# Kernel tuning notes

Hardware: AMD Instinct MI355X
Metric: run time of the kernel (lower is better)

Reference implementation:

```python
import jax, jax.numpy as jnp
import numpy as np

N_TOKEN = 100000
D = 1024  # d_embed == d_model == d_proj
CUTOFFS = [0, 20000, 60000, 100000]  # cutoff_ends
N_SEQ = 2048


def setup_inputs() -> dict:
    key = jax.random.key(0)
    ks = jax.random.split(key, 20)
    w = lambda k, s: jax.random.normal(k, s, dtype=jnp.float32) * 0.02
    return {
        "x": jax.random.randint(ks[0], (N_SEQ,), 0, N_TOKEN),
        "labels": jax.random.randint(ks[1], (N_SEQ,), 0, N_TOKEN),
        # adaptive embedding tables (d_emb_i = 1024 / 4**i) and projections [d_proj, d_emb_i]
        "emb_w0": w(ks[2], (20000, 1024)),
        "emb_w1": w(ks[3], (40000, 256)),
        "emb_w2": w(ks[4], (40000, 64)),
        "emb_proj0": w(ks[5], (1024, 1024)),
        "emb_proj1": w(ks[6], (1024, 256)),
        "emb_proj2": w(ks[7], (1024, 64)),
        # adaptive softmax output layers + projections
        "out_w0": w(ks[8], (20000, 1024)),
        "out_b0": jnp.zeros((20000,), jnp.float32),
        "out_w1": w(ks[9], (40000, 256)),
        "out_b1": jnp.zeros((40000,), jnp.float32),
        "out_w2": w(ks[10], (40000, 64)),
        "out_b2": jnp.zeros((40000,), jnp.float32),
        "out_proj0": w(ks[11], (1024, 1024)),
        "out_proj1": w(ks[12], (1024, 256)),
        "out_proj2": w(ks[13], (1024, 64)),
        # cluster head tokens (one per tail cluster)
        "cluster_w": w(ks[14], (2, 1024)),
        "cluster_b": jnp.zeros((2,), jnp.float32),
    }


def _forward(x, labels,
             emb_w0, emb_w1, emb_w2, emb_proj0, emb_proj1, emb_proj2,
             out_w0, out_b0, out_w1, out_b1, out_w2, out_b2,
             out_proj0, out_proj1, out_proj2, cluster_w, cluster_b):
    scale = jnp.asarray(D ** 0.5, jnp.float32)
    # AdaptiveEmbedding (div_val>1): per-cluster embed -> project to d_proj, scatter by range.
    # Equivalent vectorized form: build the full projected table once, then gather.
    table = jnp.concatenate([
        emb_w0 @ emb_proj0.T,   # [20000, D]
        emb_w1 @ emb_proj1.T,   # [40000, D]
        emb_w2 @ emb_proj2.T,   # [40000, D]
    ], axis=0)                   # [N_TOKEN, D]
    hidden = table[x] * scale    # [N, D]

    n = hidden.shape[0]
    rows = jnp.arange(n)

    # Head: cluster-0 vocab + one logit per tail cluster.
    head_w = jnp.concatenate([out_w0, cluster_w], axis=0)   # [20002, D]
    head_b = jnp.concatenate([out_b0, cluster_b], axis=0)   # [20002]
    head_logit = (hidden @ out_proj0) @ head_w.T + head_b   # [N, 20002]
    head_lp = jax.nn.log_softmax(head_logit, axis=-1)
    head_size = head_lp.shape[1]

    # Cluster 0: direct lookup in the head.
    lp0 = head_lp[rows, jnp.clip(labels, 0, CUTOFFS[1] - 1)]

    # Tail clusters: dense per-cluster log-softmax, gathered at shifted target,
    # plus the head cluster-token logprob (original TXL uses column -i).
    def tail(w, b, proj, i):
        l, r = CUTOFFS[i], CUTOFFS[i + 1]
        tail_lp = jax.nn.log_softmax((hidden @ proj) @ w.T + b, axis=-1)  # [N, r-l]
        t = jnp.clip(labels - l, 0, r - l - 1)
        return head_lp[:, head_size - i] + tail_lp[rows, t]

    lp1 = tail(out_w1, out_b1, out_proj1, 1)
    lp2 = tail(out_w2, out_b2, out_proj2, 2)

    logprob = jnp.where(labels < CUTOFFS[1], lp0,
               jnp.where(labels < CUTOFFS[2], lp1, lp2))
    return -logprob  # nll, [N]


def reference(x, labels,
              emb_w0, emb_w1, emb_w2, emb_proj0, emb_proj1, emb_proj2,
              out_w0, out_b0, out_w1, out_b1, out_w2, out_b2,
              out_proj0, out_proj1, out_proj2, cluster_w, cluster_b):
    return _forward(x, labels,
                    emb_w0, emb_w1, emb_w2, emb_proj0, emb_proj1, emb_proj2,
                    out_w0, out_b0, out_w1, out_b1, out_w2, out_b2,
                    out_proj0, out_proj1, out_proj2, cluster_w, cluster_b)
```

## Files before the change

### kernel.cpp

```cpp
#include <hip/hip_runtime.h>

typedef _Float16 f16x8 __attribute__((ext_vector_type(8)));
typedef _Float16 f16x4 __attribute__((ext_vector_type(4)));
typedef float f32x4 __attribute__((ext_vector_type(4)));
typedef int i32x8 __attribute__((ext_vector_type(8)));
typedef unsigned char u8;

#define DEVI __device__ __forceinline__

constexpr int NROWS = 2048;
constexpr int HEADV = 20002;
constexpr int HEADP = 20480;
constexpr int NCBH  = 160;
constexpr int PSTH  = 160;
constexpr int VT    = 40000;
constexpr int VTP   = 40320;
constexpr int NCBT  = 315;
constexpr int PSTT  = 320;

DEVI void glds16(const void* g, void* l) {
  __builtin_amdgcn_global_load_lds((const __attribute__((address_space(1))) unsigned int*)g,
                                   (__attribute__((address_space(3))) unsigned int*)l,
                                   16, 0, 0);
}

#define SIG(r) (((r) >> 1) & 7)

DEVI unsigned int to_e4m3(float f) {
  unsigned u = __float_as_uint(f);
  unsigned s = (u >> 24) & 0x80u;
  float a = fabsf(f);
  if (!(a < 448.f)) return s | 0x7E;
  if (a < 0.00097656f) return s;
  int exp = (int)((u >> 23) & 0xFF) - 127;
  int qexp = exp < -6 ? -6 : exp;
  int n = __float2int_rn(a * exp2f((float)(3 - qexp)));
  if (n >= 16) { qexp++; n = 8; }
  return s | (unsigned)(n < 8 ? n : (((qexp + 7) << 3) | (n - 8)));
}

DEVI float fr8(unsigned b) {
  unsigned e = (b >> 3) & 15u, m = b & 7u;
  float v;
  if (e) v = __uint_as_float(((e + 120u) << 23) | (m << 20));
  else   v = (float)m * 0.001953125f;
  return (b & 0x80u) ? -v : v;
}

__global__ void prep_par(const int* __restrict__ x, const int* __restrict__ labels,
                         int* cl, int* headcol, int* tailpos, int* pos1, int* pos2,
                         int* L1, int* L2, int* T0, int* T1, int* T2, int* counts)
{
  int n = blockIdx.x * 256 + threadIdx.x;
  int l = labels[n];
  int c = l < 20000 ? 0 : (l < 60000 ? 1 : 2);
  cl[n] = c;
  headcol[n] = c == 0 ? l : (c == 1 ? 20001 : 20000);
  tailpos[n] = c == 1 ? l - 20000 : (c == 2 ? l - 60000 : 0);
  if (c == 1) { int s = atomicAdd(&counts[0], 1); pos1[n] = s; L1[s] = n; }
  else if (c == 2) { int s = atomicAdd(&counts[1], 1); pos2[n] = s; L2[s] = n; }
  int t = x[n];
  int tc = t < 20000 ? 0 : (t < 60000 ? 1 : 2);
  int s = atomicAdd(&counts[2 + tc], 1);
  (tc == 0 ? T0 : tc == 1 ? T1 : T2)[s] = n;
}

constexpr int PB_A = HEADP * 1024 / 8 / 256;
constexpr int PB_B = PB_A + VTP * 256 / 8 / 256;
constexpr int PB_C = PB_B + VTP * 128 / 8 / 256;
constexpr int PB_D = PB_C + 1024;
constexpr int PB_E = PB_D + 256;
constexpr int PB_F = PB_E + 64;
constexpr int PB_G = PB_F + 1024;
constexpr int PB_H = PB_G + 256;
constexpr int PB_I = PB_H + 128;

DEVI void cvt_f16(const float* src, _Float16* dst, int vb, int tid) {
  int g = vb * 256 + tid;
  float4 v = *(const float4*)(src + (size_t)g * 4);
  f16x4 o = {(_Float16)v.x, (_Float16)v.y, (_Float16)v.z, (_Float16)v.w};
  *(f16x4*)(dst + (size_t)g * 4) = o;
}

DEVI void tr32(const float* in, _Float16* out, int C, int bx, int by, int tid) {
  __shared__ float tile[32][33];
  int c0 = bx * 32, r0 = by * 32;
  int tx = tid & 31, ty = tid >> 5;
  for (int i = 0; i < 4; i++) {
    int c = c0 + tx; int r = r0 + ty + i * 8;
    tile[ty + i * 8][tx] = (c < C) ? in[(size_t)r * C + c] : 0.f;
  }
  __syncthreads();
  for (int i = 0; i < 4; i++)
    out[(size_t)(c0 + ty + i * 8) * 1024 + r0 + tx] = (_Float16)tile[tx][ty + i * 8];
}

DEVI unsigned long pack8(const float* v) {
  unsigned long p = 0;
  #pragma unroll
  for (int j = 0; j < 8; j++) p |= (unsigned long)to_e4m3(v[j] * 64.f) << (8 * j);
  return p;
}

__global__ void fused_pack(const float* __restrict__ out_w0, const float* __restrict__ out_b0,
                           const float* __restrict__ cluster_w, const float* __restrict__ cluster_b,
                           const float* __restrict__ out_w1, const float* __restrict__ out_b1,
                           const float* __restrict__ out_w2, const float* __restrict__ out_b2,
                           const float* __restrict__ emb_proj0, const float* __restrict__ emb_proj1,
                           const float* __restrict__ emb_proj2,
                           const float* __restrict__ out_proj0, const float* __restrict__ out_proj1,
                           const float* __restrict__ out_proj2,
                           u8* headw, float* headb,
                           u8* w1q, float* b1p, u8* w2q, float* b2p,
                           _Float16* ep0f, _Float16* ep1f, _Float16* ep2f,
                           _Float16* op0T, _Float16* op1T, _Float16* op2T,
                           int* lists, int* counts)
{
  int bid = blockIdx.x, tid = threadIdx.x;
  int zi = bid * 256 + tid;
  if (zi < 5 * 2048) lists[zi] = 0;
  if (bid == 41 && tid < 8) counts[tid] = 0;
  if (bid < PB_A) {
    int g = bid * 256 + tid;
    int r = g >> 7, sl = g & 127;
    float v[8] = {};
    if (r < 20000) {
      *(float4*)v = *(const float4*)(out_w0 + (size_t)r * 1024 + sl * 8);
      *(float4*)(v + 4) = *(const float4*)(out_w0 + (size_t)r * 1024 + sl * 8 + 4);
    } else if (r < 20002) {
      *(float4*)v = *(const float4*)(cluster_w + (size_t)(r - 20000) * 1024 + sl * 8);
      *(float4*)(v + 4) = *(const float4*)(cluster_w + (size_t)(r - 20000) * 1024 + sl * 8 + 4);
    }
    *(unsigned long*)(headw + (size_t)r * 1024 + ((sl ^ SIG(r)) << 3)) = pack8(v);
    if (g < HEADP) headb[g] = g < 20000 ? out_b0[g] : (g < HEADV ? cluster_b[g - 20000] : -1e30f);
  } else if (bid < PB_B) {
    int g = (bid - PB_A) * 256 + tid;
    int r = g >> 5, sl = g & 31;
    float v[8] = {};
    if (r < VT) {
      *(float4*)v = *(const float4*)(out_w1 + (size_t)r * 256 + sl * 8);
      *(float4*)(v + 4) = *(const float4*)(out_w1 + (size_t)r * 256 + sl * 8 + 4);
    }
    *(unsigned long*)(w1q + (size_t)r * 256 + ((sl ^ SIG(r)) << 3)) = pack8(v);
    if (g < VTP) b1p[g] = g < VT ? out_b1[g] : -1e30f;
  } else if (bid < PB_C) {
    int g = (bid - PB_B) * 256 + tid;
    int r = g >> 4, sl = g & 15;
    float v[8] = {};
    if (r < VT && sl < 8) {
      *(float4*)v = *(const float4*)(out_w2 + (size_t)r * 64 + sl * 8);
      *(float4*)(v + 4) = *(const float4*)(out_w2 + (size_t)r * 64 + sl * 8 + 4);
    }
    *(unsigned long*)(w2q + (size_t)r * 128 + ((sl ^ SIG(r)) << 3)) = pack8(v);
    if (g < VTP) b2p[g] = g < VT ? out_b2[g] : -1e30f;
  } else if (bid < PB_D) { cvt_f16(emb_proj0, ep0f, bid - PB_C, tid); }
  else if (bid < PB_E) { cvt_f16(emb_proj1, ep1f, bid - PB_D, tid); }
  else if (bid < PB_F) { cvt_f16(emb_proj2, ep2f, bid - PB_E, tid); }
  else if (bid < PB_G) { int l = bid - PB_F; tr32(out_proj0, op0T, 1024, l & 31, l >> 5, tid); }
  else if (bid < PB_H) { int l = bid - PB_G; tr32(out_proj1, op1T, 256, l & 7, l >> 3, tid); }
  else                 { int l = bid - PB_H; tr32(out_proj2, op2T, 64, l & 3, l >> 2, tid); }
}

DEVI void gat(const float* emb, const int* x, const int* list, _Float16* dst,
              int tbase, int vmax, int log2E, int vb, int tid) {
  int g = vb * 256 + tid;
  int r = g >> (log2E - 2);
  int e4 = (g & ((1 << (log2E - 2)) - 1)) << 2;
  int n = list[r];
  int tl = x[n] - tbase;
  tl = tl < 0 ? 0 : (tl >= vmax ? vmax - 1 : tl);
  float4 v = *(const float4*)(emb + ((size_t)tl << log2E) + e4);
  f16x4 o = {(_Float16)(v.x * 32.f), (_Float16)(v.y * 32.f),
             (_Float16)(v.z * 32.f), (_Float16)(v.w * 32.f)};
  *(f16x4*)(dst + ((size_t)r << log2E) + e4) = o;
}

__global__ void fused_gather(const float* __restrict__ emb_w0, const float* __restrict__ emb_w1,
                             const float* __restrict__ emb_w2, const int* __restrict__ x,
                             const int* __restrict__ T0, const int* __restrict__ T1,
                             const int* __restrict__ T2,
                             _Float16* E0, _Float16* E1, _Float16* E2)
{
  int bid = blockIdx.x, tid = threadIdx.x;
  if (bid < 2048)      gat(emb_w0, x, T0, E0, 0, 20000, 10, bid, tid);
  else if (bid < 2560) gat(emb_w1, x, T1, E1, 20000, 40000, 8, bid - 2048, tid);
  else                 gat(emb_w2, x, T2, E2, 60000, 40000, 6, bid - 2560, tid);
}

struct Seg128 {
  const _Float16* A; int lda;
  const _Float16* Wm; int ldw;
  _Float16* C; int ldc; int Nvalid;
  u8* Cq; int ldq;
  const int* amap; const int* cmap; const int* cnt;
  int K; int nblk;
};

DEVI void gemm128_body(const Seg128& s, int rb, int cb) {
  int valid = s.cnt ? *s.cnt : NROWS;
  if (rb * 128 >= valid) return;
  __shared__ __attribute__((aligned(16))) _Float16 As[128 * 32];
  __shared__ __attribute__((aligned(16))) _Float16 Ws[128 * 32];
  int tid = threadIdx.x;
  int lane = tid & 63, wid = tid >> 6;
  int wr = wid >> 1, wc = wid & 1;
  int sr = wid * 32 + (lane >> 2);
  int arow0 = rb * 128 + sr, arow1 = arow0 + 16;
  if (s.amap) { arow0 = s.amap[arow0]; arow1 = s.amap[arow1]; }
  int ko = (lane & 3) * 8;
  const _Float16* ag0 = s.A + (size_t)arow0 * s.lda + ko;
  const _Float16* ag1 = s.A + (size_t)arow1 * s.lda + ko;
  const _Float16* wg0 = s.Wm + (size_t)(cb * 128 + sr) * s.ldw + ko;
  const _Float16* wg1 = wg0 + (size_t)16 * s.ldw;
  _Float16* as0 = As + (wid * 32) * 32;
  _Float16* as1 = as0 + 16 * 32;
  _Float16* ws0 = Ws + (wid * 32) * 32;
  _Float16* ws1 = ws0 + 16 * 32;
  f32x4 acc[4][4] = {};
  int lr = lane & 15, lk = (lane >> 4) * 8;
  const int nk = s.K >> 5;
  for (int kt = 0; kt < nk; ++kt) {
    int kofs = kt * 32;
    glds16(ag0 + kofs, as0);
    glds16(ag1 + kofs, as1);
    glds16(wg0 + kofs, ws0);
    glds16(wg1 + kofs, ws1);
    __syncthreads();
    f16x8 af[4], bf[4];
    #pragma unroll
    for (int mi = 0; mi < 4; mi++)
      af[mi] = *(const f16x8*)(As + (wr * 64 + mi * 16 + lr) * 32 + lk);
    #pragma unroll
    for (int ni = 0; ni < 4; ni++)
      bf[ni] = *(const f16x8*)(Ws + (wc * 64 + ni * 16 + lr) * 32 + lk);
    #pragma unroll
    for (int mi = 0; mi < 4; mi++)
      #pragma unroll
      for (int ni = 0; ni < 4; ni++)
        acc[mi][ni] = __builtin_amdgcn_mfma_f32_16x16x32_f16(af[mi], bf[ni], acc[mi][ni], 0, 0, 0);
    __syncthreads();
  }
  #pragma unroll
  for (int mi = 0; mi < 4; mi++) {
    #pragma unroll
    for (int j = 0; j < 4; j++) {
      int rl = wr * 64 + mi * 16 + (lane >> 4) * 4 + j;
      int rg = rb * 128 + rl;
      if (rg >= valid) continue;
      int orow = s.cmap ? s.cmap[rg] : rg;
      #pragma unroll
      for (int ni = 0; ni < 4; ni++) {
        int col = cb * 128 + wc * 64 + ni * 16 + (lane & 15);
        if (col < s.Nvalid) {
          float v = acc[mi][ni][j];
          s.C[(size_t)orow * s.ldc + col] = (_Float16)v;
          if (s.Cq) {
            int sl = col >> 3;
            s.Cq[(size_t)orow * s.ldq + (((sl ^ SIG(orow)) << 3) | (col & 7))] = (u8)to_e4m3(v * 8.f);
          }
        }
      }
    }
  }
}

__global__ __launch_bounds__(256)
void gemm128_multi(Seg128 s0, Seg128 s1, Seg128 s2) {
  int b = blockIdx.x;
  if (b < s0.nblk)                    { gemm128_body(s0, b & 15, b >> 4); }
  else if (b < s0.nblk + s1.nblk)     { b -= s0.nblk; gemm128_body(s1, b & 15, b >> 4); }
  else                                { b -= s0.nblk + s1.nblk; gemm128_body(s2, b & 15, b >> 4); }
}

struct SegL {
  const u8* A; const u8* W; const float* bias; const int* cnt;
  float* pm; float* ps; int pstride; int K; int nrb; int nblk;
};

__global__ __launch_bounds__(256)
void gemm_lse8_multi(SegL s0, SegL s1, SegL s2)
{
  __shared__ __attribute__((aligned(16))) u8 As[16384];
  __shared__ __attribute__((aligned(16))) u8 Ws[16384];

  int b = blockIdx.x;
  SegL s;
  if (b < s0.nblk) s = s0;
  else if (b < s0.nblk + s1.nblk) { s = s1; b -= s0.nblk; }
  else { s = s2; b -= s0.nblk + s1.nblk; }

  int q = s.nblk >> 3;
  int w = (b & 7) * q + (b >> 3);
  int rb = w % s.nrb, cb = w / s.nrb;
  int valid = s.cnt ? *s.cnt : NROWS;
  if (rb * 128 >= valid) return;

  const int K = s.K;
  int tid = threadIdx.x;
  int lane = tid & 63, wid = tid >> 6;
  int wr = wid >> 1, wc = wid & 1;
  int lr = lane & 15, g = lane >> 4;

  const u8* aS[4]; const u8* bS[4]; int dL[4];
  #pragma unroll
  for (int i = 0; i < 4; ++i) {
    int c = tid + i * 256;
    int r = c >> 3, j = c & 7;
    aS[i] = s.A + (size_t)(rb * 128 + r) * K + j * 16;
    bS[i] = s.W + (size_t)((size_t)cb * 128 + r) * K + j * 16;
    dL[i] = c * 16;
  }

  int sig = (lr >> 1) & 7;
  int o0 = ((g * 4 + 0) ^ sig) << 3;
  int o1 = ((g * 4 + 1) ^ sig) << 3;
  int o2 = ((g * 4 + 2) ^ sig) << 3;
  int o3 = ((g * 4 + 3) ^ sig) << 3;
  int arow = (wr * 64 + lr) * 128;
  int brow = (wc * 64 + lr) * 128;

  f32x4 acc[4][4] = {};
  const int nk = K >> 7;

  union UV { i32x8 v; long l[4]; };
  for (int kt = 0; kt < nk; ++kt) {
    int k0 = kt * 128;
    #pragma unroll
    for (int i = 0; i < 4; ++i) glds16(aS[i] + k0, As + dL[i]);
    #pragma unroll
    for (int i = 0; i < 4; ++i) glds16(bS[i] + k0, Ws + dL[i]);
    __syncthreads();
    i32x8 bq[4];
    #pragma unroll
    for (int ni = 0; ni < 4; ++ni) {
      UV bv;
      const u8* bp = Ws + brow + ni * 2048;
      bv.l[0] = *(const long*)(bp + o0);
      bv.l[1] = *(const long*)(bp + o1);
      bv.l[2] = *(const long*)(bp + o2);
      bv.l[3] = *(const long*)(bp + o3);
      bq[ni] = bv.v;
    }
    #pragma unroll
    for (int mi = 0; mi < 4; ++mi) {
      UV av;
      const u8* ap = As + arow + mi * 2048;
      av.l[0] = *(const long*)(ap + o0);
      av.l[1] = *(const long*)(ap + o1);
      av.l[2] = *(const long*)(ap + o2);
      av.l[3] = *(const long*)(ap + o3);
      #pragma unroll
      for (int ni = 0; ni < 4; ++ni)
        acc[mi][ni] = __builtin_amdgcn_mfma_scale_f32_16x16x128_f8f6f4(
                        av.v, bq[ni], acc[mi][ni], 0, 0, 0, 127, 0, 127);
    }
    __syncthreads();
  }

  float* lm = (float*)As;
  float* lsm = lm + 256;
  float bv4[4];
  #pragma unroll
  for (int ni = 0; ni < 4; ++ni) bv4[ni] = s.bias[cb * 128 + wc * 64 + ni * 16 + lr];
  constexpr float INV = 1.f / 512.f;
  #pragma unroll
  for (int mi = 0; mi < 4; ++mi) {
    #pragma unroll
    for (int j = 0; j < 4; ++j) {
      float v0 = acc[mi][0][j] * INV + bv4[0];
      float v1 = acc[mi][1][j] * INV + bv4[1];
      float v2 = acc[mi][2][j] * INV + bv4[2];
      float v3 = acc[mi][3][j] * INV + bv4[3];
      float m = fmaxf(fmaxf(v0, v1), fmaxf(v2, v3));
      #pragma unroll
      for (int d = 1; d < 16; d <<= 1) m = fmaxf(m, __shfl_xor(m, d));
      float sm = __expf(v0 - m) + __expf(v1 - m) + __expf(v2 - m) + __expf(v3 - m);
      #pragma unroll
      for (int d = 1; d < 16; d <<= 1) sm += __shfl_xor(sm, d);
      if (lr == 0) {
        int row = wr * 64 + mi * 16 + g * 4 + j;
        lm[wc * 128 + row] = m; lsm[wc * 128 + row] = sm;
      }
    }
  }
  __syncthreads();
  if (tid < 128) {
    float m0 = lm[tid], m1 = lm[128 + tid];
    float M = fmaxf(m0, m1);
    float S = lsm[tid] * __expf(m0 - M) + lsm[128 + tid] * __expf(m1 - M);
    int gr = rb * 128 + tid;
    s.pm[(size_t)gr * s.pstride + cb] = M;
    s.ps[(size_t)gr * s.pstride + cb] = S;
  }
}

DEVI float lsew(const float* m, const float* s, int nb, int lane) {
  float M = -3e38f;
  for (int i = lane; i < nb; i += 64) M = fmaxf(M, m[i]);
  #pragma unroll
  for (int d = 1; d < 64; d <<= 1) M = fmaxf(M, __shfl_xor(M, d));
  float S = 0.f;
  for (int i = lane; i < nb; i += 64) S += s[i] * __expf(m[i] - M);
  #pragma unroll
  for (int d = 1; d < 64; d <<= 1) S += __shfl_xor(S, d);
  return M + __logf(S);
}

__global__ void finish_kernel(const _Float16* __restrict__ ph0, const u8* __restrict__ headw,
                              const float* __restrict__ headb,
                              const _Float16* __restrict__ ph1c, const u8* __restrict__ w1q,
                              const float* __restrict__ b1p,
                              const _Float16* __restrict__ ph2c, const u8* __restrict__ w2q,
                              const float* __restrict__ b2p,
                              const int* __restrict__ headcol, const int* __restrict__ tailpos,
                              const int* __restrict__ pos1, const int* __restrict__ pos2,
                              const int* __restrict__ cl,
                              const float* __restrict__ pmh, const float* __restrict__ psh,
                              const float* __restrict__ pm1, const float* __restrict__ ps1,
                              const float* __restrict__ pm2, const float* __restrict__ ps2,
                              float* __restrict__ out)
{
  int n = blockIdx.x;
  int tid = threadIdx.x, lane = tid & 63, wid = tid >> 6;
  __shared__ float sh[6];
  int c = cl[n];
  constexpr float IW = 1.f / 64.f;
  if (wid == 0) {
    int hc = headcol[n];
    const f16x8* a = (const f16x8*)(ph0 + (size_t)n * 1024 + lane * 16);
    float s = 0.f;
    #pragma unroll
    for (int u = 0; u < 2; u++) {
      int sl = lane * 2 + u;
      unsigned long wq = *(const unsigned long*)(headw + (size_t)hc * 1024 + (((sl ^ SIG(hc)) << 3)));
      f16x8 av = a[u];
      #pragma unroll
      for (int j = 0; j < 8; j++) s += (float)av[j] * fr8((unsigned)(wq >> (8 * j)) & 0xFFu);
    }
    #pragma unroll
    for (int d = 1; d < 64; d <<= 1) s += __shfl_xor(s, d);
    if (lane == 0) sh[0] = s * IW + headb[hc];
  } else if (wid == 1 && c == 1) {
    int p = pos1[n], t = tailpos[n];
    f16x4 av = *(const f16x4*)(ph1c + (size_t)p * 256 + lane * 4);
    int sl = lane >> 1;
    const u8* ww = w1q + (size_t)t * 256 + ((sl ^ SIG(t)) << 3) + (lane & 1) * 4;
    float s = (float)av[0] * fr8(ww[0]) + (float)av[1] * fr8(ww[1])
            + (float)av[2] * fr8(ww[2]) + (float)av[3] * fr8(ww[3]);
    #pragma unroll
    for (int d = 1; d < 64; d <<= 1) s += __shfl_xor(s, d);
    float l = lsew(pm1 + (size_t)p * PSTT, ps1 + (size_t)p * PSTT, NCBT, lane);
    if (lane == 0) { sh[1] = s * IW + b1p[t]; sh[4] = l; }
  } else if (wid == 2 && c == 2) {
    int p = pos2[n], t = tailpos[n];
    const _Float16* a = ph2c + (size_t)p * 128 + lane * 2;
    int sl = lane >> 2;
    const u8* ww = w2q + (size_t)t * 128 + ((sl ^ SIG(t)) << 3) + (lane & 3) * 2;
    float s = (float)a[0] * fr8(ww[0]) + (float)a[1] * fr8(ww[1]);
    #pragma unroll
    for (int d = 1; d < 64; d <<= 1) s += __shfl_xor(s, d);
    float l = lsew(pm2 + (size_t)p * PSTT, ps2 + (size_t)p * PSTT, NCBT, lane);
    if (lane == 0) { sh[2] = s * IW + b2p[t]; sh[5] = l; }
  } else if (wid == 3) {
    float l = lsew(pmh + (size_t)n * PSTH, psh + (size_t)n * PSTH, NCBH, lane);
    if (lane == 0) sh[3] = l;
  }
  __syncthreads();
  if (tid == 0) {
    float nll = sh[3] - sh[0];
    if (c == 1)      nll += sh[4] - sh[1];
    else if (c == 2) nll += sh[5] - sh[2];
    out[n] = nll;
  }
}

extern "C" void kernel_launch(void* const* d_in, const int* in_sizes, int n_in,
                              void* d_out, int out_size, void* d_ws, size_t ws_size,
                              hipStream_t stream)
{
  const int*   x         = (const int*)d_in[0];
  const int*   labels    = (const int*)d_in[1];
  const float* emb_w0    = (const float*)d_in[2];
  const float* emb_w1    = (const float*)d_in[3];
  const float* emb_w2    = (const float*)d_in[4];
  const float* emb_proj0 = (const float*)d_in[5];
  const float* emb_proj1 = (const float*)d_in[6];
  const float* emb_proj2 = (const float*)d_in[7];
  const float* out_w0    = (const float*)d_in[8];
  const float* out_b0    = (const float*)d_in[9];
  const float* out_w1    = (const float*)d_in[10];
  const float* out_b1    = (const float*)d_in[11];
  const float* out_w2    = (const float*)d_in[12];
  const float* out_b2    = (const float*)d_in[13];
  const float* out_proj0 = (const float*)d_in[14];
  const float* out_proj1 = (const float*)d_in[15];
  const float* out_proj2 = (const float*)d_in[16];
  const float* cluster_w = (const float*)d_in[17];
  const float* cluster_b = (const float*)d_in[18];
  float* out = (float*)d_out;

  char* ws = (char*)d_ws;
  size_t off = 0;
  auto alloc = [&](size_t bytes) -> void* {
    void* p = ws + off;
    off = (off + bytes + 255) & ~(size_t)255;
    return p;
  };
  u8*    headw = (u8*)alloc((size_t)HEADP * 1024);
  float* headb = (float*)alloc((size_t)HEADP * 4);
  u8*    w1q   = (u8*)alloc((size_t)VTP * 256);
  float* b1p   = (float*)alloc((size_t)VTP * 4);
  u8*    w2q   = (u8*)alloc((size_t)VTP * 128);
  float* b2p   = (float*)alloc((size_t)VTP * 4);
  _Float16* ep0f = (_Float16*)alloc((size_t)1024 * 1024 * 2);
  _Float16* ep1f = (_Float16*)alloc((size_t)1024 * 256 * 2);
  _Float16* ep2f = (_Float16*)alloc((size_t)1024 * 64 * 2);
  _Float16* op0T = (_Float16*)alloc((size_t)1024 * 1024 * 2);
  _Float16* op1T = (_Float16*)alloc((size_t)256 * 1024 * 2);
  _Float16* op2T = (_Float16*)alloc((size_t)128 * 1024 * 2);
  _Float16* E0   = (_Float16*)alloc((size_t)NROWS * 1024 * 2);
  _Float16* E1   = (_Float16*)alloc((size_t)NROWS * 256 * 2);
  _Float16* E2   = (_Float16*)alloc((size_t)NROWS * 64 * 2);
  _Float16* hid  = (_Float16*)alloc((size_t)NROWS * 1024 * 2);
  _Float16* ph0  = (_Float16*)alloc((size_t)NROWS * 1024 * 2);
  u8*       ph0q = (u8*)alloc((size_t)NROWS * 1024);
  _Float16* ph1c = (_Float16*)alloc((size_t)NROWS * 256 * 2);
  u8*       ph1q = (u8*)alloc((size_t)NROWS * 256);
  _Float16* ph2c = (_Float16*)alloc((size_t)NROWS * 128 * 2);
  u8*       ph2q = (u8*)alloc((size_t)NROWS * 128);
  float* pmh = (float*)alloc((size_t)NROWS * PSTH * 4);
  float* psh = (float*)alloc((size_t)NROWS * PSTH * 4);
  float* pm1 = (float*)alloc((size_t)NROWS * PSTT * 4);
  float* ps1 = (float*)alloc((size_t)NROWS * PSTT * 4);
  float* pm2 = (float*)alloc((size_t)NROWS * PSTT * 4);
  float* ps2 = (float*)alloc((size_t)NROWS * PSTT * 4);
  int* lists = (int*)alloc(5 * NROWS * 4);
  int* L1 = lists;
  int* L2 = lists + 2048;
  int* T0 = lists + 4096;
  int* T1 = lists + 6144;
  int* T2 = lists + 8192;
  int* counts  = (int*)alloc(16 * 4);
  int* cl      = (int*)alloc(NROWS * 4);
  int* headcol = (int*)alloc(NROWS * 4);
  int* tailpos = (int*)alloc(NROWS * 4);
  int* pos1    = (int*)alloc(NROWS * 4);
  int* pos2    = (int*)alloc(NROWS * 4);
  (void)ws_size; (void)in_sizes; (void)n_in; (void)out_size;

  fused_pack<<<PB_I, 256, 0, stream>>>(out_w0, out_b0, cluster_w, cluster_b,
                                       out_w1, out_b1, out_w2, out_b2,
                                       emb_proj0, emb_proj1, emb_proj2,
                                       out_proj0, out_proj1, out_proj2,
                                       headw, headb, w1q, b1p, w2q, b2p,
                                       ep0f, ep1f, ep2f, op0T, op1T, op2T,
                                       lists, counts);

  prep_par<<<8, 256, 0, stream>>>(x, labels, cl, headcol, tailpos, pos1, pos2,
                                  L1, L2, T0, T1, T2, counts);

  fused_gather<<<2688, 256, 0, stream>>>(emb_w0, emb_w1, emb_w2, x, T0, T1, T2, E0, E1, E2);

  Seg128 h0 = {E0, 1024, ep0f, 1024, hid, 1024, 1024, nullptr, 0, nullptr, T0, counts + 2, 1024, 128};
  Seg128 h1 = {E1, 256,  ep1f, 256,  hid, 1024, 1024, nullptr, 0, nullptr, T1, counts + 3, 256,  128};
  Seg128 h2 = {E2, 64,   ep2f, 64,   hid, 1024, 1024, nullptr, 0, nullptr, T2, counts + 4, 64,   128};
  gemm128_multi<<<384, 256, 0, stream>>>(h0, h1, h2);

  Seg128 p0 = {hid, 1024, op0T, 1024, ph0,  1024, 1024, ph0q, 1024, nullptr, nullptr, nullptr,   1024, 128};
  Seg128 p1 = {hid, 1024, op1T, 1024, ph1c, 256,  256,  ph1q, 256,  L1,      nullptr, counts + 0, 1024, 32};
  Seg128 p2 = {hid, 1024, op2T, 1024, ph2c, 128,  128,  ph2q, 128,  L2,      nullptr, counts + 1, 1024, 16};
  gemm128_multi<<<176, 256, 0, stream>>>(p0, p1, p2);

  SegL l0 = {ph0q, headw, headb, nullptr,    pmh, psh, PSTH, 1024, 16, 16 * NCBH};
  SegL l1 = {ph1q, w1q,   b1p,   counts + 0, pm1, ps1, PSTT, 256,  8,  8 * NCBT};
  SegL l2 = {ph2q, w2q,   b2p,   counts + 1, pm2, ps2, PSTT, 128,  8,  8 * NCBT};
  gemm_lse8_multi<<<16 * NCBH + 16 * NCBT, 256, 0, stream>>>(l0, l1, l2);

  finish_kernel<<<NROWS, 256, 0, stream>>>(ph0, headw, headb, ph1c, w1q, b1p,
                                           ph2c, w2q, b2p, headcol, tailpos, pos1, pos2, cl,
                                           pmh, psh, pm1, ps1, pm2, ps2, out);
}
```

Before: 314.8 us.

## Switch FP8 swizzle to 16-byte granules and use 128-bit LDS reads

Changes the XOR swizzle on the FP8 weight and activation buffers from 8-byte to 16-byte granules within each 128-byte chunk. The FP8 GEMM can then fetch each MFMA operand with two 128-bit LDS loads instead of four 64-bit loads. The layout is updated in the writer, the GEMM and the gather kernels so they stay consistent. It also adds a minimum-occupancy hint of 3 blocks per SM to the launch bounds, which may force register spilling.

```diff
diff --git a/kernel.cpp b/kernel.cpp
--- a/kernel.cpp
+++ b/kernel.cpp
@@ -3,6 +3,7 @@
 typedef _Float16 f16x8 __attribute__((ext_vector_type(8)));
 typedef _Float16 f16x4 __attribute__((ext_vector_type(4)));
 typedef float f32x4 __attribute__((ext_vector_type(4)));
+typedef int i32x4 __attribute__((ext_vector_type(4)));
 typedef int i32x8 __attribute__((ext_vector_type(8)));
 typedef unsigned char u8;
 
@@ -25,6 +26,9 @@
 }
 
 #define SIG(r) (((r) >> 1) & 7)
+DEVI int swzb(int b, int r) {
+  return (b & ~127) | ((((b >> 4) & 7) ^ SIG(r)) << 4) | (b & 15);
+}
 
 DEVI unsigned int to_e4m3(float f) {
   unsigned u = __float_as_uint(f);
@@ -131,7 +135,7 @@
       *(float4*)v = *(const float4*)(cluster_w + (size_t)(r - 20000) * 1024 + sl * 8);
       *(float4*)(v + 4) = *(const float4*)(cluster_w + (size_t)(r - 20000) * 1024 + sl * 8 + 4);
     }
-    *(unsigned long*)(headw + (size_t)r * 1024 + ((sl ^ SIG(r)) << 3)) = pack8(v);
+    *(unsigned long*)(headw + (size_t)r * 1024 + swzb(sl * 8, r)) = pack8(v);
     if (g < HEADP) headb[g] = g < 20000 ? out_b0[g] : (g < HEADV ? cluster_b[g - 20000] : -1e30f);
   } else if (bid < PB_B) {
     int g = (bid - PB_A) * 256 + tid;
@@ -141,7 +145,7 @@
       *(float4*)v = *(const float4*)(out_w1 + (size_t)r * 256 + sl * 8);
       *(float4*)(v + 4) = *(const float4*)(out_w1 + (size_t)r * 256 + sl * 8 + 4);
     }
-    *(unsigned long*)(w1q + (size_t)r * 256 + ((sl ^ SIG(r)) << 3)) = pack8(v);
+    *(unsigned long*)(w1q + (size_t)r * 256 + swzb(sl * 8, r)) = pack8(v);
     if (g < VTP) b1p[g] = g < VT ? out_b1[g] : -1e30f;
   } else if (bid < PB_C) {
     int g = (bid - PB_B) * 256 + tid;
@@ -151,7 +155,7 @@
       *(float4*)v = *(const float4*)(out_w2 + (size_t)r * 64 + sl * 8);
       *(float4*)(v + 4) = *(const float4*)(out_w2 + (size_t)r * 64 + sl * 8 + 4);
     }
-    *(unsigned long*)(w2q + (size_t)r * 128 + ((sl ^ SIG(r)) << 3)) = pack8(v);
+    *(unsigned long*)(w2q + (size_t)r * 128 + swzb(sl * 8, r)) = pack8(v);
     if (g < VTP) b2p[g] = g < VT ? out_b2[g] : -1e30f;
   } else if (bid < PB_D) { cvt_f16(emb_proj0, ep0f, bid - PB_C, tid); }
   else if (bid < PB_E) { cvt_f16(emb_proj1, ep1f, bid - PB_D, tid); }
@@ -254,10 +258,7 @@
         if (col < s.Nvalid) {
           float v = acc[mi][ni][j];
           s.C[(size_t)orow * s.ldc + col] = (_Float16)v;
-          if (s.Cq) {
-            int sl = col >> 3;
-            s.Cq[(size_t)orow * s.ldq + (((sl ^ SIG(orow)) << 3) | (col & 7))] = (u8)to_e4m3(v * 8.f);
-          }
+          if (s.Cq) s.Cq[(size_t)orow * s.ldq + swzb(col, orow)] = (u8)to_e4m3(v * 8.f);
         }
       }
     }
@@ -277,7 +278,7 @@
   float* pm; float* ps; int pstride; int K; int nrb; int nblk;
 };
 
-__global__ __launch_bounds__(256)
+__global__ __launch_bounds__(256, 3)
 void gemm_lse8_multi(SegL s0, SegL s1, SegL s2)
 {
   __shared__ __attribute__((aligned(16))) u8 As[16384];
@@ -311,18 +312,16 @@
     dL[i] = c * 16;
   }
 
-  int sig = (lr >> 1) & 7;
-  int o0 = ((g * 4 + 0) ^ sig) << 3;
-  int o1 = ((g * 4 + 1) ^ sig) << 3;
-  int o2 = ((g * 4 + 2) ^ sig) << 3;
-  int o3 = ((g * 4 + 3) ^ sig) << 3;
+  int sig = SIG(lr);
+  int p0 = ((2 * g + 0) ^ sig) << 4;
+  int p1 = ((2 * g + 1) ^ sig) << 4;
   int arow = (wr * 64 + lr) * 128;
   int brow = (wc * 64 + lr) * 128;
 
   f32x4 acc[4][4] = {};
   const int nk = K >> 7;
 
-  union UV { i32x8 v; long l[4]; };
+  union UV { i32x8 v; i32x4 h[2]; };
   for (int kt = 0; kt < nk; ++kt) {
     int k0 = kt * 128;
     #pragma unroll
@@ -335,20 +334,16 @@
     for (int ni = 0; ni < 4; ++ni) {
       UV bv;
       const u8* bp = Ws + brow + ni * 2048;
-      bv.l[0] = *(const long*)(bp + o0);
-      bv.l[1] = *(const long*)(bp + o1);
-      bv.l[2] = *(const long*)(bp + o2);
-      bv.l[3] = *(const long*)(bp + o3);
+      bv.h[0] = *(const i32x4*)(bp + p0);
+      bv.h[1] = *(const i32x4*)(bp + p1);
       bq[ni] = bv.v;
     }
     #pragma unroll
     for (int mi = 0; mi < 4; ++mi) {
       UV av;
       const u8* ap = As + arow + mi * 2048;
-      av.l[0] = *(const long*)(ap + o0);
-      av.l[1] = *(const long*)(ap + o1);
-      av.l[2] = *(const long*)(ap + o2);
-      av.l[3] = *(const long*)(ap + o3);
+      av.h[0] = *(const i32x4*)(ap + p0);
+      av.h[1] = *(const i32x4*)(ap + p1);
       #pragma unroll
       for (int ni = 0; ni < 4; ++ni)
         acc[mi][ni] = __builtin_amdgcn_mfma_scale_f32_16x16x128_f8f6f4(
@@ -431,8 +426,7 @@
     float s = 0.f;
     #pragma unroll
     for (int u = 0; u < 2; u++) {
-      int sl = lane * 2 + u;
-      unsigned long wq = *(const unsigned long*)(headw + (size_t)hc * 1024 + (((sl ^ SIG(hc)) << 3)));
+      unsigned long wq = *(const unsigned long*)(headw + (size_t)hc * 1024 + swzb(lane * 16 + u * 8, hc));
       f16x8 av = a[u];
       #pragma unroll
       for (int j = 0; j < 8; j++) s += (float)av[j] * fr8((unsigned)(wq >> (8 * j)) & 0xFFu);
@@ -443,8 +437,7 @@
   } else if (wid == 1 && c == 1) {
     int p = pos1[n], t = tailpos[n];
     f16x4 av = *(const f16x4*)(ph1c + (size_t)p * 256 + lane * 4);
-    int sl = lane >> 1;
-    const u8* ww = w1q + (size_t)t * 256 + ((sl ^ SIG(t)) << 3) + (lane & 1) * 4;
+    const u8* ww = w1q + (size_t)t * 256 + swzb(lane * 4, t);
     float s = (float)av[0] * fr8(ww[0]) + (float)av[1] * fr8(ww[1])
             + (float)av[2] * fr8(ww[2]) + (float)av[3] * fr8(ww[3]);
     #pragma unroll
@@ -454,8 +447,7 @@
   } else if (wid == 2 && c == 2) {
     int p = pos2[n], t = tailpos[n];
     const _Float16* a = ph2c + (size_t)p * 128 + lane * 2;
-    int sl = lane >> 2;
-    const u8* ww = w2q + (size_t)t * 128 + ((sl ^ SIG(t)) << 3) + (lane & 3) * 2;
+    const u8* ww = w2q + (size_t)t * 128 + swzb(lane * 2, t);
     float s = (float)a[0] * fr8(ww[0]) + (float)a[1] * fr8(ww[1]);
     #pragma unroll
     for (int d = 1; d < 64; d <<= 1) s += __shfl_xor(s, d);
```

New measurement: 255.4 us. -18.9%, faster.
